# Kernel tuning notes

Measured on AMD Instinct MI355X. Metric: run time of the kernel, lower is better.

## Reference

```python
import jax, jax.numpy as jnp
import numpy as np

B, L, E = 2, 2048, 2048
H, KVH, HD = 16, 4, 128          # n_heads, n_kv_heads, head_dim = E // H
WIN = 512                        # window_size
SCALE = 1.0 / (HD ** 0.5)
NEG = -1e30


def setup_inputs() -> dict:
    key = jax.random.key(0)
    ks = jax.random.split(key, 5)
    s = 0.02
    return {
        "x":  jax.random.normal(ks[0], (B, L, E), dtype=jnp.float32),
        "Wq": jax.random.normal(ks[1], (E, H * HD), dtype=jnp.float32) * s,
        "Wk": jax.random.normal(ks[2], (E, KVH * HD), dtype=jnp.float32) * s,
        "Wv": jax.random.normal(ks[3], (E, KVH * HD), dtype=jnp.float32) * s,
        "Wo": jax.random.normal(ks[4], (H * HD, E), dtype=jnp.float32) * s,
    }


def reference(x, Wq, Wk, Wv, Wo):
    # projections
    q = (x @ Wq).reshape(B, L, H, HD)      # [B, L, H, HD]
    k = (x @ Wk).reshape(B, L, KVH, HD)    # [B, L, KVH, HD]
    v = (x @ Wv).reshape(B, L, KVH, HD)
    # GQA: expand kv heads (repeat_interleave over head dim)
    rep = H // KVH
    k = jnp.repeat(k, rep, axis=2)         # [B, L, H, HD]
    v = jnp.repeat(v, rep, axis=2)
    # scores [B, H, L, L]
    scores = jnp.einsum("bqhd,bkhd->bhqk", q, k) * SCALE
    i = jnp.arange(L)[:, None]
    j = jnp.arange(L)[None, :]
    mask = (j > i) | (j < i - WIN)         # True = masked
    scores = jnp.where(mask[None, None], NEG, scores)
    attn = jax.nn.softmax(scores, axis=-1)
    out = jnp.einsum("bhqk,bkhd->bqhd", attn, v).reshape(B, L, H * HD)
    return out @ Wo                        # [B, L, E]
```

## Files before the change

kernel.cpp:

```cpp
#include <hip/hip_runtime.h>
#include <hip/hip_bf16.h>
#include <type_traits>

#define B_ 2
#define L_ 2048
#define E_ 2048
#define H_ 16
#define KVH_ 4
#define HD_ 128
#define WIN_ 512
#define REP_ (H_ / KVH_)
#define SCALE_ 0.08838834764831843f

typedef __bf16 bf16x8 __attribute__((ext_vector_type(8)));
typedef float f32x4 __attribute__((ext_vector_type(4)));
typedef unsigned short u16x8 __attribute__((ext_vector_type(8)));

__device__ __forceinline__ unsigned short f2bf(float x) {
    __hip_bfloat16 h = __float2bfloat16(x);
    return *reinterpret_cast<unsigned short*>(&h);
}

__device__ __forceinline__ void gload_lds16(const unsigned short* g, unsigned short* l) {
    __builtin_amdgcn_global_load_lds(
        (const __attribute__((address_space(1))) void*)g,
        (__attribute__((address_space(3))) void*)l,
        16, 0, 0);
}

__global__ __launch_bounds__(256) void conv_f32_bf16(
        const float* __restrict__ in, unsigned short* __restrict__ out, int n4) {
    int i = blockIdx.x * 256 + threadIdx.x;
    if (i >= n4) return;
    float4 v = reinterpret_cast<const float4*>(in)[i];
    ushort4 o;
    o.x = f2bf(v.x); o.y = f2bf(v.y); o.z = f2bf(v.z); o.w = f2bf(v.w);
    reinterpret_cast<ushort4*>(out)[i] = o;
}

__global__ __launch_bounds__(256) void transpose_f32_bf16(
        const float* __restrict__ W, unsigned short* __restrict__ WT,
        int K, int N, int wts) {
    __shared__ unsigned short tile[32][33];
    const int t = threadIdx.x;
    const int r = t >> 5, c = t & 31;
    const int k0 = blockIdx.y * 32, n0 = blockIdx.x * 32;
    #pragma unroll
    for (int i = 0; i < 4; ++i)
        tile[r + i * 8][c] = f2bf(W[(size_t)(k0 + r + i * 8) * N + n0 + c]);
    __syncthreads();
    #pragma unroll
    for (int i = 0; i < 4; ++i)
        WT[(size_t)(n0 + r + i * 8) * wts + k0 + c] = tile[c][r + i * 8];
}

__global__ __launch_bounds__(256) void transpose_v_bf16(
        const unsigned short* __restrict__ kv, unsigned short* __restrict__ vT) {
    __shared__ unsigned short tile[32][33];
    const int t = threadIdx.x;
    const int r = t >> 5, c = t & 31;
    const int l0 = blockIdx.y * 32;
    const int n0 = blockIdx.x * 32;
    #pragma unroll
    for (int i = 0; i < 4; ++i)
        tile[r + i * 8][c] = kv[(size_t)(l0 + r + i * 8) * 1024 + 512 + n0 + c];
    __syncthreads();
    const int bq = l0 >> 11, lqv = l0 & 2047;
    #pragma unroll
    for (int i = 0; i < 4; ++i)
        vT[(size_t)(bq * 512 + n0 + r + i * 8) * (size_t)L_ + lqv + c] = tile[c][r + i * 8];
}

template<typename OT>
__global__ __launch_bounds__(256) void gemm_bt(
        const unsigned short* __restrict__ A, const unsigned short* __restrict__ BT,
        OT* __restrict__ C, int M, int N, int K) {
    __shared__ __attribute__((aligned(16))) unsigned short As[128 * 32];
    __shared__ __attribute__((aligned(16))) unsigned short Bs[128 * 32];
    const int t  = threadIdx.x;
    const int wv = t >> 6, ln = t & 63;
    const int wr = wv >> 1, wc = wv & 1;
    const int bm = blockIdx.y * 128, bn = blockIdx.x * 128;
    const int lrow = ln & 15;
    const int lk8  = (ln >> 4) * 8;

    f32x4 acc[4][4];
    const f32x4 z = {0.f, 0.f, 0.f, 0.f};
    #pragma unroll
    for (int m = 0; m < 4; ++m)
        #pragma unroll
        for (int n = 0; n < 4; ++n) acc[m][n] = z;

    for (int k0 = 0; k0 < K; k0 += 32) {
        #pragma unroll
        for (int seg = 0; seg < 2; ++seg) {
            const int chunk = seg * 256 + t;
            const int row = chunk >> 2, c8 = (chunk & 3) * 8;
            const int lbase = (seg * 256 + wv * 64) * 8;
            gload_lds16(A  + (size_t)(bm + row) * K + k0 + c8, &As[lbase]);
            gload_lds16(BT + (size_t)(bn + row) * K + k0 + c8, &Bs[lbase]);
        }
        __syncthreads();
        bf16x8 af[4], bfr[4];
        #pragma unroll
        for (int m = 0; m < 4; ++m)
            af[m] = *reinterpret_cast<const bf16x8*>(
                &As[(wr * 64 + m * 16 + lrow) * 32 + lk8]);
        #pragma unroll
        for (int n = 0; n < 4; ++n)
            bfr[n] = *reinterpret_cast<const bf16x8*>(
                &Bs[(wc * 64 + n * 16 + lrow) * 32 + lk8]);
        #pragma unroll
        for (int m = 0; m < 4; ++m)
            #pragma unroll
            for (int n = 0; n < 4; ++n)
                acc[m][n] = __builtin_amdgcn_mfma_f32_16x16x32_bf16(
                    af[m], bfr[n], acc[m][n], 0, 0, 0);
        __syncthreads();
    }
    const int crq = (ln >> 4) * 4;
    #pragma unroll
    for (int m = 0; m < 4; ++m)
        #pragma unroll
        for (int n = 0; n < 4; ++n)
            #pragma unroll
            for (int r = 0; r < 4; ++r) {
                size_t idx = (size_t)(bm + wr * 64 + m * 16 + crq + r) * N
                             + bn + wc * 64 + n * 16 + lrow;
                if constexpr (std::is_same_v<OT, float>) C[idx] = acc[m][n][r];
                else C[idx] = f2bf(acc[m][n][r]);
            }
}

__global__ __launch_bounds__(256) void attn_mfma(
        const unsigned short* __restrict__ qb,
        const unsigned short* __restrict__ kvb,
        const unsigned short* __restrict__ vT,
        unsigned short* __restrict__ ob) {
    __shared__ __attribute__((aligned(16))) unsigned short Ks[32 * 128];
    __shared__ __attribute__((aligned(16))) unsigned short VsT[128 * 40];
    __shared__ __bf16 Pl[4][32][17];

    const int t  = threadIdx.x;
    const int w  = t >> 6, l = t & 63;
    const int bh = blockIdx.y;
    const int b  = bh >> 4, h = bh & 15;
    const int kh = h >> 2;
    const int i0 = blockIdx.x * 64;
    const int iw = i0 + w * 16;
    const int lq = l & 15;
    const int g  = l >> 4;
    const int g8 = g * 8;
    const int i  = iw + lq;

    bf16x8 qf[4];
    {
        const unsigned short* qrow = qb + (size_t)(b * L_ + iw + lq) * E_ + h * HD_;
        #pragma unroll
        for (int dc = 0; dc < 4; ++dc)
            qf[dc] = *reinterpret_cast<const bf16x8*>(qrow + dc * 32 + g8);
    }

    f32x4 oacc[8];
    const f32x4 z = {0.f, 0.f, 0.f, 0.f};
    #pragma unroll
    for (int c = 0; c < 8; ++c) oacc[c] = z;
    float mreg = -50000.f, lreg = 0.f;

    int jlo = i0 - WIN_; if (jlo < 0) jlo = 0;
    const int nch = (i0 + 64 - jlo) >> 5;
    const int wlo = iw - WIN_, whi = iw + 15;
    const unsigned short* vbase = vT + (size_t)((b * KVH_ + kh) * HD_) * L_;

    for (int ch = 0; ch < nch; ++ch) {
        const int jb = jlo + ch * 32;
        #pragma unroll
        for (int s = 0; s < 2; ++s) {
            const int e  = t + s * 256;
            const int kr = e >> 4;
            const int d8 = (e & 15) * 8;
            u16x8 kk = *reinterpret_cast<const u16x8*>(
                kvb + (size_t)(b * L_ + jb + kr) * 1024 + kh * HD_ + d8);
            *reinterpret_cast<u16x8*>(&Ks[kr * 128 + (d8 ^ ((kr & 7) << 3))]) = kk;
            const int dv = e >> 2;
            const int k8 = (e & 3) * 8;
            u16x8 vv = *reinterpret_cast<const u16x8*>(
                vbase + (size_t)dv * L_ + jb + k8);
            *reinterpret_cast<u16x8*>(&VsT[dv * 40 + k8]) = vv;
        }
        __syncthreads();

        if (jb + 31 >= wlo && jb <= whi) {
            f32x4 st[2]; st[0] = z; st[1] = z;
            #pragma unroll
            for (int kt = 0; kt < 2; ++kt) {
                const int krow = kt * 16 + lq;
                #pragma unroll
                for (int dc = 0; dc < 4; ++dc) {
                    bf16x8 kf = *reinterpret_cast<const bf16x8*>(
                        &Ks[krow * 128 + ((dc * 32 + g8) ^ ((krow & 7) << 3))]);
                    st[kt] = __builtin_amdgcn_mfma_f32_16x16x32_bf16(
                        kf, qf[dc], st[kt], 0, 0, 0);
                }
            }
            float p8[2][4];
            float cmax = -1e30f;
            #pragma unroll
            for (int kt = 0; kt < 2; ++kt)
                #pragma unroll
                for (int r = 0; r < 4; ++r) {
                    const int j = jb + kt * 16 + g * 4 + r;
                    float s = st[kt][r] * SCALE_;
                    s = (j <= i && j >= i - WIN_) ? s : -1e30f;
                    p8[kt][r] = s;
                    cmax = fmaxf(cmax, s);
                }
            cmax = fmaxf(cmax, __shfl_xor(cmax, 16));
            cmax = fmaxf(cmax, __shfl_xor(cmax, 32));
            const float mnew  = fmaxf(mreg, cmax);
            const float alpha = __expf(mreg - mnew);
            float psum = 0.f;
            #pragma unroll
            for (int kt = 0; kt < 2; ++kt)
                #pragma unroll
                for (int r = 0; r < 4; ++r) {
                    const float p = __expf(p8[kt][r] - mnew);
                    p8[kt][r] = p; psum += p;
                }
            psum += __shfl_xor(psum, 16);
            psum += __shfl_xor(psum, 32);
            lreg = lreg * alpha + psum;
            mreg = mnew;
            #pragma unroll
            for (int kt = 0; kt < 2; ++kt)
                #pragma unroll
                for (int r = 0; r < 4; ++r)
                    Pl[w][kt * 16 + g * 4 + r][lq] = (__bf16)p8[kt][r];
            bf16x8 pb;
            #pragma unroll
            for (int j = 0; j < 8; ++j) pb[j] = Pl[w][g8 + j][lq];
            #pragma unroll
            for (int c = 0; c < 8; ++c)
                #pragma unroll
                for (int r = 0; r < 4; ++r) oacc[c][r] *= alpha;
            #pragma unroll
            for (int c = 0; c < 8; ++c) {
                bf16x8 af = *reinterpret_cast<const bf16x8*>(
                    &VsT[(c * 16 + lq) * 40 + g8]);
                oacc[c] = __builtin_amdgcn_mfma_f32_16x16x32_bf16(
                    af, pb, oacc[c], 0, 0, 0);
            }
        }
        __syncthreads();
    }

    const float inv = 1.f / lreg;
    unsigned short* orow = ob + (size_t)(b * L_ + iw + lq) * E_ + h * HD_;
    #pragma unroll
    for (int c = 0; c < 8; ++c) {
        ushort4 o4;
        o4.x = f2bf(oacc[c][0] * inv);
        o4.y = f2bf(oacc[c][1] * inv);
        o4.z = f2bf(oacc[c][2] * inv);
        o4.w = f2bf(oacc[c][3] * inv);
        *reinterpret_cast<ushort4*>(&orow[c * 16 + g * 4]) = o4;
    }
}

extern "C" void kernel_launch(void* const* d_in, const int* in_sizes, int n_in,
                              void* d_out, int out_size, void* d_ws, size_t ws_size,
                              hipStream_t stream) {
    const float* x  = (const float*)d_in[0];
    const float* Wq = (const float*)d_in[1];
    const float* Wk = (const float*)d_in[2];
    const float* Wv = (const float*)d_in[3];
    const float* Wo = (const float*)d_in[4];
    float* out = (float*)d_out;

    const int M = B_ * L_;
    char* w = (char*)d_ws;
    unsigned short* qbuf  = (unsigned short*)w; w += (size_t)M * E_ * 2;
    unsigned short* kvbuf = (unsigned short*)w; w += (size_t)M * 1024 * 2;
    unsigned short* xb    = (unsigned short*)w; w += (size_t)M * E_ * 2;
    unsigned short* wT1   = (unsigned short*)w; w += (size_t)E_ * E_ * 2;
    unsigned short* wkvT  = (unsigned short*)w; w += (size_t)1024 * E_ * 2;
    unsigned short* vTb   = (unsigned short*)w; w += (size_t)1024 * L_ * 2;

    dim3 blk(256);

    conv_f32_bf16<<<dim3((M * E_ / 4 + 255) / 256), blk, 0, stream>>>(x, xb, M * E_ / 4);
    transpose_f32_bf16<<<dim3(E_ / 32, E_ / 32), blk, 0, stream>>>(Wq, wT1, E_, E_, E_);
    transpose_f32_bf16<<<dim3(512 / 32, E_ / 32), blk, 0, stream>>>(Wk, wkvT, E_, 512, E_);
    transpose_f32_bf16<<<dim3(512 / 32, E_ / 32), blk, 0, stream>>>(Wv, wkvT + (size_t)512 * E_, E_, 512, E_);

    gemm_bt<unsigned short><<<dim3(E_ / 128, M / 128), blk, 0, stream>>>(
        xb, wT1, qbuf, M, E_, E_);
    gemm_bt<unsigned short><<<dim3(1024 / 128, M / 128), blk, 0, stream>>>(
        xb, wkvT, kvbuf, M, 1024, E_);

    transpose_v_bf16<<<dim3(512 / 32, M / 32), blk, 0, stream>>>(kvbuf, vTb);

    attn_mfma<<<dim3(L_ / 64, B_ * H_), blk, 0, stream>>>(qbuf, kvbuf, vTb, xb);

    transpose_f32_bf16<<<dim3(E_ / 32, E_ / 32), blk, 0, stream>>>(Wo, wT1, E_, E_, E_);
    gemm_bt<float><<<dim3(E_ / 128, M / 128), blk, 0, stream>>>(xb, wT1, out, M, E_, E_);
}
```

Measured before the change: 366.2 us.

## Remap workgroups, add MFMA priority, lazy softmax rescale, shuffle-based P transpose

The GEMM remaps its workgroup index in chunks of eight, which appears aimed at placing neighbouring tiles on the same XCD for L2 reuse. It also raises wave priority around the MFMA loops. The attention kernel orders query tiles heaviest-first using an XCD-aware mapping and skips the online-softmax rescale when the max grows by at most 8. It also replaces the LDS round-trip for the P fragment transpose with cross-lane shuffles. Together these target cache locality, load balance, exp/multiply work and LDS traffic. In exchange, the grid mapping in attention hardcodes 1024 workgroups, and the lazy rescale allows values up to e^8 before renormalising.

```diff
diff --git a/kernel.cpp b/kernel.cpp
--- a/kernel.cpp
+++ b/kernel.cpp
@@ -80,7 +80,10 @@
     const int t  = threadIdx.x;
     const int wv = t >> 6, ln = t & 63;
     const int wr = wv >> 1, wc = wv & 1;
-    const int bm = blockIdx.y * 128, bn = blockIdx.x * 128;
+    const int nwg = gridDim.x * gridDim.y;
+    int lin = blockIdx.y * gridDim.x + blockIdx.x;
+    if ((nwg & 7) == 0) lin = (lin & 7) * (nwg >> 3) + (lin >> 3);
+    const int bm = (lin / gridDim.x) * 128, bn = (lin % gridDim.x) * 128;
     const int lrow = ln & 15;
     const int lk8  = (ln >> 4) * 8;
 
@@ -110,12 +113,14 @@
         for (int n = 0; n < 4; ++n)
             bfr[n] = *reinterpret_cast<const bf16x8*>(
                 &Bs[(wc * 64 + n * 16 + lrow) * 32 + lk8]);
+        __builtin_amdgcn_s_setprio(1);
         #pragma unroll
         for (int m = 0; m < 4; ++m)
             #pragma unroll
             for (int n = 0; n < 4; ++n)
                 acc[m][n] = __builtin_amdgcn_mfma_f32_16x16x32_bf16(
                     af[m], bfr[n], acc[m][n], 0, 0, 0);
+        __builtin_amdgcn_s_setprio(0);
         __syncthreads();
     }
     const int crq = (ln >> 4) * 4;
@@ -139,14 +144,16 @@
         unsigned short* __restrict__ ob) {
     __shared__ __attribute__((aligned(16))) unsigned short Ks[32 * 128];
     __shared__ __attribute__((aligned(16))) unsigned short VsT[128 * 40];
-    __shared__ __bf16 Pl[4][32][17];
 
     const int t  = threadIdx.x;
     const int w  = t >> 6, l = t & 63;
-    const int bh = blockIdx.y;
+    const int lin = blockIdx.y * gridDim.x + blockIdx.x;
+    const int wid = (lin & 7) * 128 + (lin >> 3);
+    const int bh  = wid >> 5;
+    const int qt  = 31 - (wid & 31);
     const int b  = bh >> 4, h = bh & 15;
     const int kh = h >> 2;
-    const int i0 = blockIdx.x * 64;
+    const int i0 = qt * 64;
     const int iw = i0 + w * 16;
     const int lq = l & 15;
     const int g  = l >> 4;
@@ -192,6 +199,7 @@
 
         if (jb + 31 >= wlo && jb <= whi) {
             f32x4 st[2]; st[0] = z; st[1] = z;
+            __builtin_amdgcn_s_setprio(1);
             #pragma unroll
             for (int kt = 0; kt < 2; ++kt) {
                 const int krow = kt * 16 + lq;
@@ -203,6 +211,7 @@
                         kf, qf[dc], st[kt], 0, 0, 0);
                 }
             }
+            __builtin_amdgcn_s_setprio(0);
             float p8[2][4];
             float cmax = -1e30f;
             #pragma unroll
@@ -217,32 +226,46 @@
                 }
             cmax = fmaxf(cmax, __shfl_xor(cmax, 16));
             cmax = fmaxf(cmax, __shfl_xor(cmax, 32));
-            const float mnew  = fmaxf(mreg, cmax);
-            const float alpha = __expf(mreg - mnew);
+            const bool noresc = __all(cmax - mreg <= 8.f);
+            float alpha = 1.f;
+            if (!noresc) {
+                const float mnew = fmaxf(mreg, cmax);
+                alpha = __expf(mreg - mnew);
+                mreg = mnew;
+            }
             float psum = 0.f;
             #pragma unroll
             for (int kt = 0; kt < 2; ++kt)
                 #pragma unroll
                 for (int r = 0; r < 4; ++r) {
-                    const float p = __expf(p8[kt][r] - mnew);
+                    const float p = __expf(p8[kt][r] - mreg);
                     p8[kt][r] = p; psum += p;
                 }
             psum += __shfl_xor(psum, 16);
             psum += __shfl_xor(psum, 32);
-            lreg = lreg * alpha + psum;
-            mreg = mnew;
-            #pragma unroll
-            for (int kt = 0; kt < 2; ++kt)
+            if (noresc) {
+                lreg += psum;
+            } else {
+                lreg = lreg * alpha + psum;
                 #pragma unroll
-                for (int r = 0; r < 4; ++r)
-                    Pl[w][kt * 16 + g * 4 + r][lq] = (__bf16)p8[kt][r];
-            bf16x8 pb;
-            #pragma unroll
-            for (int j = 0; j < 8; ++j) pb[j] = Pl[w][g8 + j][lq];
-            #pragma unroll
-            for (int c = 0; c < 8; ++c)
-                #pragma unroll
-                for (int r = 0; r < 4; ++r) oacc[c][r] *= alpha;
+                for (int c = 0; c < 8; ++c)
+                    #pragma unroll
+                    for (int r = 0; r < 4; ++r) oacc[c][r] *= alpha;
+            }
+            const unsigned u00 = ((unsigned)f2bf(p8[0][1]) << 16) | f2bf(p8[0][0]);
+            const unsigned u01 = ((unsigned)f2bf(p8[0][3]) << 16) | f2bf(p8[0][2]);
+            const unsigned u10 = ((unsigned)f2bf(p8[1][1]) << 16) | f2bf(p8[1][0]);
+            const unsigned u11 = ((unsigned)f2bf(p8[1][3]) << 16) | f2bf(p8[1][2]);
+            union { unsigned u[4]; bf16x8 v; } pu;
+            #pragma unroll
+            for (int wd = 0; wd < 4; ++wd) {
+                const int src = ((g & 1) * 2 + (wd >> 1)) * 16 + lq;
+                const unsigned a0 = __shfl(wd & 1 ? u01 : u00, src);
+                const unsigned a1 = __shfl(wd & 1 ? u11 : u10, src);
+                pu.u[wd] = (g < 2) ? a0 : a1;
+            }
+            const bf16x8 pb = pu.v;
+            __builtin_amdgcn_s_setprio(1);
             #pragma unroll
             for (int c = 0; c < 8; ++c) {
                 bf16x8 af = *reinterpret_cast<const bf16x8*>(
@@ -250,6 +273,7 @@
                 oacc[c] = __builtin_amdgcn_mfma_f32_16x16x32_bf16(
                     af, pb, oacc[c], 0, 0, 0);
             }
+            __builtin_amdgcn_s_setprio(0);
         }
         __syncthreads();
     }
```

After: 344.5 us. -5.9%, faster.
